# Kernel optimization log

Measured on AMD Instinct MI355X. Metric: run time of the kernel, lower is better.

The kernel has to match this reference:

```python
import jax, jax.numpy as jnp
import numpy as np
from jax import lax

B, IN_CH, OUT_CH, K, STYLE_DIM, H, W = 4, 512, 512, 3, 512, 64, 64


def setup_inputs() -> dict:
    key = jax.random.key(0)
    ks = jax.random.split(key, 6)
    x = jax.random.normal(ks[0], (B, B * IN_CH, H, W), dtype=jnp.float32)
    style = jax.random.normal(ks[1], (B, STYLE_DIM), dtype=jnp.float32)
    # learned params
    weight = jax.random.normal(ks[2], (1, OUT_CH, IN_CH, K, K), dtype=jnp.float32)
    demod = jnp.ones((1, OUT_CH, 1, 1), dtype=jnp.float32)
    # nn.Linear(style_dim, in_channels): kaiming-uniform-ish init approximated
    lim = 1.0 / np.sqrt(STYLE_DIM)
    mod_w = jax.random.uniform(ks[3], (IN_CH, STYLE_DIM), minval=-lim, maxval=lim, dtype=jnp.float32)
    mod_b = jax.random.uniform(ks[4], (IN_CH,), minval=-lim, maxval=lim, dtype=jnp.float32)
    return {"x": x, "style": style, "weight": weight, "demod": demod, "mod_w": mod_w, "mod_b": mod_b}


def reference(x, style, weight, demod, mod_w, mod_b):
    b = x.shape[0]
    out_ch, in_ch, k = weight.shape[1], weight.shape[2], weight.shape[3]
    # style modulation: Linear(style) -> (B, in_ch) -> (B,1,in_ch,1,1)
    s = style @ mod_w.T + mod_b
    w = weight * s[:, None, :, None, None]          # (B, out, in, k, k)
    # demod (1,out,1,1) broadcasts against trailing (in,k,k) axes -> needs out==in (as in torch)
    w = w * demod
    w = w.reshape(b * out_ch, in_ch, k, k)           # OIHW grouped kernel
    pad = k // 2
    out = lax.conv_general_dilated(
        x, w,
        window_strides=(1, 1),
        padding=[(pad, pad), (pad, pad)],
        dimension_numbers=("NCHW", "OIHW", "NCHW"),
        feature_group_count=b,
    )
    return out  # (B, B*out_ch, H, W)
```

## Files before the change

kernel.cpp:

```cpp
#include <hip/hip_runtime.h>

typedef __attribute__((ext_vector_type(4))) float f32x4;
typedef __attribute__((ext_vector_type(8))) short bf16x8;
typedef unsigned long long u64;
typedef unsigned short u16;
typedef unsigned int u32;

static __device__ __forceinline__ u16 f2bf(float f) {
    u32 u = __float_as_uint(f);
    u += 0x7fffu + ((u >> 16) & 1u);
    return (u16)(u >> 16);
}

__global__ void k_style(const float* __restrict__ style, const float* __restrict__ mod_w,
                        const float* __restrict__ mod_b, float* __restrict__ s_ws) {
    int t = blockIdx.x * 256 + threadIdx.x;
    int g = t >> 9, ic = t & 511;
    const f32x4* st = (const f32x4*)(style + (g << 9));
    const f32x4* mw = (const f32x4*)(mod_w + (ic << 9));
    float acc = 0.f;
#pragma unroll 4
    for (int d = 0; d < 128; ++d) {
        f32x4 a = st[d], b = mw[d];
        acc += a[0]*b[0] + a[1]*b[1] + a[2]*b[2] + a[3]*b[3];
    }
    s_ws[t] = acc + mod_b[ic];
}

__global__ void k_wmod(const float* __restrict__ weight, const float* __restrict__ demod,
                       const float* __restrict__ s_ws, short* __restrict__ wmod) {
    int t = blockIdx.x * 256 + threadIdx.x;
    int ic = t & 511, oc = (t >> 9) & 511, g = t >> 18;
    float sv = s_ws[(g << 9) + ic] * demod[ic];
    const float* wp = weight + ((size_t)((oc << 9) + ic)) * 9;
#pragma unroll
    for (int tap = 0; tap < 9; ++tap) {
        size_t idx = ((size_t)((g * 9 + tap) * 512 + oc) << 9) + ic;
        wmod[idx] = (short)f2bf(wp[tap] * sv);
    }
}

__global__ __launch_bounds__(256, 2) void k_conv(const float* __restrict__ x,
                                                 const short* __restrict__ wmod,
                                                 float* __restrict__ out) {
    __shared__ __align__(16) short Xs[396 * 64];
    __shared__ __align__(16) short Ws[128 * 64];

    const int tid  = threadIdx.x;
    const int lane = tid & 63;
    const int wv   = tid >> 6;
    const int wr   = wv >> 1, wc = wv & 1;
    const int l15  = lane & 15;
    const int l4   = lane >> 4;
    const int rowb = blockIdx.x & 15, ocb = blockIdx.x >> 4;
    const int g    = blockIdx.y, nb = blockIdx.z;
    const int y0   = rowb << 2;

    const float* xg = x + (((size_t)(nb * 2048 + (g << 9))) << 12);
    const short* wg = wmod + (size_t)g * (9 * 512 * 512) + ((size_t)(ocb * 128) << 9);
    float* outg = out + (((size_t)(nb * 2048 + (g << 9) + ocb * 128)) << 12) + (rowb << 8);

    for (int i = tid; i < 6336; i += 256) ((u64*)Xs)[i] = 0ull;

    f32x4 acc[4][8];
#pragma unroll
    for (int m = 0; m < 4; ++m)
#pragma unroll
        for (int nn = 0; nn < 8; ++nn) acc[m][nn] = (f32x4){0.f, 0.f, 0.f, 0.f};

    for (int ch = 0; ch < 8; ++ch) {
        const int ic0 = ch << 6;
        __syncthreads();

        {
            const int q = tid & 15, icg4 = tid >> 4;
#pragma unroll
            for (int r = 0; r < 6; ++r) {
                const int gy = y0 - 1 + r;
                if (gy >= 0 && gy <= 63) {
                    const float* src = xg + (((size_t)(ic0 + (icg4 << 2))) << 12) + (gy << 6) + (q << 2);
                    f32x4 v0 = *(const f32x4*)(src);
                    f32x4 v1 = *(const f32x4*)(src + 4096);
                    f32x4 v2 = *(const f32x4*)(src + 8192);
                    f32x4 v3 = *(const f32x4*)(src + 12288);
                    const int pb = r * 66 + 1 + (q << 2);
#pragma unroll
                    for (int c = 0; c < 4; ++c) {
                        const int p = pb + c;
                        u64 pk = (u64)f2bf(v0[c]) | ((u64)f2bf(v1[c]) << 16)
                               | ((u64)f2bf(v2[c]) << 32) | ((u64)f2bf(v3[c]) << 48);
                        const int blk = (icg4 >> 1) ^ (p & 7);
                        *(u64*)&Xs[(p << 6) + (blk << 3) + ((icg4 & 1) << 2)] = pk;
                    }
                }
            }
        }

        for (int tap = 0; tap < 9; ++tap) {
            if (tap) __syncthreads();
#pragma unroll
            for (int it = 0; it < 4; ++it) {
                const int j = tid + (it << 8);
                const int blk = j & 7, oc = j >> 3;
                bf16x8 w8 = *(const bf16x8*)&wg[tap * 262144 + (oc << 9) + ic0 + (blk << 3)];
                *(bf16x8*)&Ws[(oc << 6) + ((blk ^ (oc & 7)) << 3)] = w8;
            }
            __syncthreads();

            const int dy = tap / 3 - 1, dx = tap % 3 - 1;
#pragma unroll
            for (int kk = 0; kk < 2; ++kk) {
                const int bblk = (kk << 2) + l4;
                bf16x8 a[4], b[8];
#pragma unroll
                for (int m = 0; m < 4; ++m) {
                    const int oc = (wr << 6) + (m << 4) + l15;
                    a[m] = *(const bf16x8*)&Ws[(oc << 6) + ((bblk ^ (oc & 7)) << 3)];
                }
#pragma unroll
                for (int nn = 0; nn < 8; ++nn) {
                    const int j = (wc << 7) + (nn << 4) + l15;
                    const int p = ((j >> 6) + 1 + dy) * 66 + (j & 63) + 1 + dx;
                    b[nn] = *(const bf16x8*)&Xs[(p << 6) + ((bblk ^ (p & 7)) << 3)];
                }
#pragma unroll
                for (int m = 0; m < 4; ++m)
#pragma unroll
                    for (int nn = 0; nn < 8; ++nn)
                        acc[m][nn] = __builtin_amdgcn_mfma_f32_16x16x32_bf16(a[m], b[nn], acc[m][nn], 0, 0, 0);
            }
        }
    }

#pragma unroll
    for (int m = 0; m < 4; ++m)
#pragma unroll
        for (int nn = 0; nn < 8; ++nn) {
            const int oc = (wr << 6) + (m << 4) + (l4 << 2);
            const int p  = (wc << 7) + (nn << 4) + l15;
            float* dst = outg + ((size_t)oc << 12) + p;
#pragma unroll
            for (int r = 0; r < 4; ++r) dst[(size_t)r << 12] = acc[m][nn][r];
        }
}

extern "C" void kernel_launch(void* const* d_in, const int* in_sizes, int n_in,
                              void* d_out, int out_size, void* d_ws, size_t ws_size,
                              hipStream_t stream) {
    const float* x      = (const float*)d_in[0];
    const float* style  = (const float*)d_in[1];
    const float* weight = (const float*)d_in[2];
    const float* demod  = (const float*)d_in[3];
    const float* mod_w  = (const float*)d_in[4];
    const float* mod_b  = (const float*)d_in[5];
    float* out = (float*)d_out;

    float* s_ws = (float*)d_ws;
    short* wmod = (short*)((char*)d_ws + 8192);

    hipLaunchKernelGGL(k_style, dim3(8), dim3(256), 0, stream, style, mod_w, mod_b, s_ws);
    hipLaunchKernelGGL(k_wmod, dim3(4096), dim3(256), 0, stream, weight, demod, s_ws, wmod);
    hipLaunchKernelGGL(k_conv, dim3(64, 4, 4), dim3(256), 0, stream, x, wmod, out);
}
```

Measured before the change: 313.7 us.

## Pre-pack weights in MFMA fragment order, load directly to registers with double-buffering

k_wmod now writes modulated weights already arranged in per-wave MFMA A-fragment order, so k_conv loads A operands straight from global memory into registers, double-buffered across taps. This removes the weight LDS stage and the per-tap __syncthreads pairs. The X tile now uses a padded 72-short row stride instead of XOR swizzling, and block order is changed so the four oc-blocks sharing an x tile are adjacent. The costs are higher register pressure from the a[2][8] buffers and more global load traffic per wave, since A-fragments are no longer shared through LDS.

```diff
diff --git a/kernel.cpp b/kernel.cpp
--- a/kernel.cpp
+++ b/kernel.cpp
@@ -30,21 +30,30 @@
 __global__ void k_wmod(const float* __restrict__ weight, const float* __restrict__ demod,
                        const float* __restrict__ s_ws, short* __restrict__ wmod) {
     int t = blockIdx.x * 256 + threadIdx.x;
-    int ic = t & 511, oc = (t >> 9) & 511, g = t >> 18;
-    float sv = s_ws[(g << 9) + ic] * demod[ic];
-    const float* wp = weight + ((size_t)((oc << 9) + ic)) * 9;
+    int lane = t & 63;
+    int r = t >> 6;
+    int frag = r & 7; r >>= 3;
+    int tap = r % 9; r /= 9;
+    int ch = r & 7; r >>= 3;
+    int wr = r & 1; r >>= 1;
+    int ocb = r & 3; int g = r >> 2;
+    int kk = frag >> 2, m = frag & 3;
+    int oc  = ocb*128 + wr*64 + m*16 + (lane & 15);
+    int ic0 = ch*64 + kk*32 + (lane >> 4)*8;
+    const float* wp = weight + (size_t)(oc*512 + ic0)*9 + tap;
+    const float* sp = s_ws + (g << 9) + ic0;
+    const float* dp = demod + ic0;
+    bf16x8 pk;
 #pragma unroll
-    for (int tap = 0; tap < 9; ++tap) {
-        size_t idx = ((size_t)((g * 9 + tap) * 512 + oc) << 9) + ic;
-        wmod[idx] = (short)f2bf(wp[tap] * sv);
-    }
+    for (int e = 0; e < 8; ++e)
+        pk[e] = (short)f2bf(wp[e*9] * (sp[e] * dp[e]));
+    ((bf16x8*)wmod)[t] = pk;
 }
 
 __global__ __launch_bounds__(256, 2) void k_conv(const float* __restrict__ x,
                                                  const short* __restrict__ wmod,
                                                  float* __restrict__ out) {
-    __shared__ __align__(16) short Xs[396 * 64];
-    __shared__ __align__(16) short Ws[128 * 64];
+    __shared__ __align__(16) short Xs[391 * 72];
 
     const int tid  = threadIdx.x;
     const int lane = tid & 63;
@@ -52,15 +61,20 @@
     const int wr   = wv >> 1, wc = wv & 1;
     const int l15  = lane & 15;
     const int l4   = lane >> 4;
-    const int rowb = blockIdx.x & 15, ocb = blockIdx.x >> 4;
+    const int ocb  = blockIdx.x & 3, rowb = blockIdx.x >> 2;
     const int g    = blockIdx.y, nb = blockIdx.z;
     const int y0   = rowb << 2;
 
-    const float* xg = x + (((size_t)(nb * 2048 + (g << 9))) << 12);
-    const short* wg = wmod + (size_t)g * (9 * 512 * 512) + ((size_t)(ocb * 128) << 9);
+    const float* xg   = x + (((size_t)(nb * 2048 + (g << 9))) << 12);
+    const short* wg   = wmod + ((size_t)((g * 4 + ocb) * 2 + wr)) * 294912;
     float* outg = out + (((size_t)(nb * 2048 + (g << 9) + ocb * 128)) << 12) + (rowb << 8);
 
-    for (int i = tid; i < 6336; i += 256) ((u64*)Xs)[i] = 0ull;
+    bf16x8 a[2][8];
+#pragma unroll
+    for (int f = 0; f < 8; ++f)
+        a[0][f] = *(const bf16x8*)&wg[f * 512 + lane * 8];
+
+    for (int i = tid; i < (391 * 72) / 4; i += 256) ((u64*)Xs)[i] = 0ull;
 
     f32x4 acc[4][8];
 #pragma unroll
@@ -68,66 +82,62 @@
 #pragma unroll
         for (int nn = 0; nn < 8; ++nn) acc[m][nn] = (f32x4){0.f, 0.f, 0.f, 0.f};
 
+    const int q = tid & 15, icg4 = tid >> 4;
+
     for (int ch = 0; ch < 8; ++ch) {
-        const int ic0 = ch << 6;
+        if (ch > 0) {
+            const short* wn = wg + (size_t)ch * 9 * 4096;
+#pragma unroll
+            for (int f = 0; f < 8; ++f)
+                a[0][f] = *(const bf16x8*)&wn[f * 512 + lane * 8];
+        }
         __syncthreads();
 
-        {
-            const int q = tid & 15, icg4 = tid >> 4;
 #pragma unroll
-            for (int r = 0; r < 6; ++r) {
-                const int gy = y0 - 1 + r;
-                if (gy >= 0 && gy <= 63) {
-                    const float* src = xg + (((size_t)(ic0 + (icg4 << 2))) << 12) + (gy << 6) + (q << 2);
-                    f32x4 v0 = *(const f32x4*)(src);
-                    f32x4 v1 = *(const f32x4*)(src + 4096);
-                    f32x4 v2 = *(const f32x4*)(src + 8192);
-                    f32x4 v3 = *(const f32x4*)(src + 12288);
-                    const int pb = r * 66 + 1 + (q << 2);
+        for (int r = 0; r < 6; ++r) {
+            const int gy = y0 - 1 + r;
+            if (gy >= 0 && gy <= 63) {
+                const float* src = xg + (((size_t)((ch << 6) + (icg4 << 2))) << 12) + (gy << 6) + (q << 2);
+                f32x4 v0 = *(const f32x4*)(src);
+                f32x4 v1 = *(const f32x4*)(src + 4096);
+                f32x4 v2 = *(const f32x4*)(src + 8192);
+                f32x4 v3 = *(const f32x4*)(src + 12288);
 #pragma unroll
-                    for (int c = 0; c < 4; ++c) {
-                        const int p = pb + c;
-                        u64 pk = (u64)f2bf(v0[c]) | ((u64)f2bf(v1[c]) << 16)
-                               | ((u64)f2bf(v2[c]) << 32) | ((u64)f2bf(v3[c]) << 48);
-                        const int blk = (icg4 >> 1) ^ (p & 7);
-                        *(u64*)&Xs[(p << 6) + (blk << 3) + ((icg4 & 1) << 2)] = pk;
-                    }
+                for (int c = 0; c < 4; ++c) {
+                    const int p = r * 65 + 1 + (q << 2) + c;
+                    u64 pk = (u64)f2bf(v0[c]) | ((u64)f2bf(v1[c]) << 16)
+                           | ((u64)f2bf(v2[c]) << 32) | ((u64)f2bf(v3[c]) << 48);
+                    *(u64*)&Xs[p * 72 + icg4 * 4] = pk;
                 }
             }
         }
+        __syncthreads();
 
+        const short* wch = wg + (size_t)ch * 9 * 4096;
+#pragma unroll
         for (int tap = 0; tap < 9; ++tap) {
-            if (tap) __syncthreads();
+            const int cur = tap & 1, nxt = cur ^ 1;
+            if (tap < 8) {
+                const short* wn = wch + (tap + 1) * 4096;
 #pragma unroll
-            for (int it = 0; it < 4; ++it) {
-                const int j = tid + (it << 8);
-                const int blk = j & 7, oc = j >> 3;
-                bf16x8 w8 = *(const bf16x8*)&wg[tap * 262144 + (oc << 9) + ic0 + (blk << 3)];
-                *(bf16x8*)&Ws[(oc << 6) + ((blk ^ (oc & 7)) << 3)] = w8;
+                for (int f = 0; f < 8; ++f)
+                    a[nxt][f] = *(const bf16x8*)&wn[f * 512 + lane * 8];
             }
-            __syncthreads();
-
             const int dy = tap / 3 - 1, dx = tap % 3 - 1;
 #pragma unroll
             for (int kk = 0; kk < 2; ++kk) {
-                const int bblk = (kk << 2) + l4;
-                bf16x8 a[4], b[8];
-#pragma unroll
-                for (int m = 0; m < 4; ++m) {
-                    const int oc = (wr << 6) + (m << 4) + l15;
-                    a[m] = *(const bf16x8*)&Ws[(oc << 6) + ((bblk ^ (oc & 7)) << 3)];
-                }
+                bf16x8 b[8];
 #pragma unroll
                 for (int nn = 0; nn < 8; ++nn) {
                     const int j = (wc << 7) + (nn << 4) + l15;
-                    const int p = ((j >> 6) + 1 + dy) * 66 + (j & 63) + 1 + dx;
-                    b[nn] = *(const bf16x8*)&Xs[(p << 6) + ((bblk ^ (p & 7)) << 3)];
+                    const int p = ((j >> 6) + 1 + dy) * 65 + 1 + (j & 63) + dx;
+                    b[nn] = *(const bf16x8*)&Xs[p * 72 + (kk * 4 + l4) * 8];
                 }
 #pragma unroll
                 for (int m = 0; m < 4; ++m)
 #pragma unroll
                     for (int nn = 0; nn < 8; ++nn)
-                        acc[m][nn] = __builtin_amdgcn_mfma_f32_16x16x32_bf16(a[m], b[nn], acc[m][nn], 0, 0, 0);
+                        acc[m][nn] = __builtin_amdgcn_mfma_f32_16x16x32_bf16(a[cur][kk * 4 + m], b[nn], acc[m][nn], 0, 0, 0);
             }
         }
     }
@@ -159,6 +169,6 @@
     short* wmod = (short*)((char*)d_ws + 8192);
 
     hipLaunchKernelGGL(k_style, dim3(8), dim3(256), 0, stream, style, mod_w, mod_b, s_ws);
-    hipLaunchKernelGGL(k_wmod, dim3(4096), dim3(256), 0, stream, weight, demod, s_ws, wmod);
+    hipLaunchKernelGGL(k_wmod, dim3(9216), dim3(256), 0, stream, weight, demod, s_ws, wmod);
     hipLaunchKernelGGL(k_conv, dim3(64, 4, 4), dim3(256), 0, stream, x, wmod, out);
 }
```

Result: slower. 593.2 us (+89.1%).
